# Optimization experiments

Measured on AMD Instinct MI355X. Metric: run time of the kernel, lower is better.

## Reference

```python
import jax, jax.numpy as jnp
import numpy as np

EPS = 1e-5

def layer_norm(x, g, b):
    m = x.mean(-1, keepdims=True)
    v = ((x - m) ** 2).mean(-1, keepdims=True)
    return (x - m) / jnp.sqrt(v + EPS) * g + b

def multihead(qn, kn, vn, Wq, Wk, Wv, causal):
    # Wq/Wk/Wv: [H, E, D]; per-head projections stacked over H (matches per-head Linear loop)
    Q = jnp.einsum('ble,hed->bhld', qn, Wq)
    K = jnp.einsum('bme,hed->bhmd', kn, Wk)
    V = jnp.einsum('bme,hed->bhmd', vn, Wv)
    scale = Q.shape[-1] ** -0.5
    s = jnp.einsum('bhld,bhmd->bhlm', Q, K) * scale
    if causal:
        L, M = s.shape[-2], s.shape[-1]
        mask = jnp.tril(jnp.ones((L, M), dtype=bool))
        s = jnp.where(mask, s, -jnp.inf)
    w = jax.nn.softmax(s, axis=-1)
    o = jnp.einsum('bhlm,bhmd->bhld', w, V)
    return o.mean(axis=1)  # heads are AVERAGED, not concatenated


def setup_inputs() -> dict:
    key = jax.random.key(0)
    ks = jax.random.split(key, 16)
    B, L, E, H, D, FW = 4, 2048, 512, 8, 512, 4
    std = 0.02
    inp = {
        'q': jax.random.normal(ks[0], (B, L, E), jnp.float32),
        'k': jax.random.normal(ks[1], (B, L, E), jnp.float32),
        'v': jax.random.normal(ks[2], (B, L, E), jnp.float32),
        'Wq_s': jax.random.normal(ks[3], (H, E, D), jnp.float32) * std,
        'Wk_s': jax.random.normal(ks[4], (H, E, D), jnp.float32) * std,
        'Wv_s': jax.random.normal(ks[5], (H, E, D), jnp.float32) * std,
        'Wq_c': jax.random.normal(ks[6], (H, E, D), jnp.float32) * std,
        'Wk_c': jax.random.normal(ks[7], (H, E, D), jnp.float32) * std,
        'Wv_c': jax.random.normal(ks[8], (H, E, D), jnp.float32) * std,
        'W1': jax.random.normal(ks[9], (E, FW * E), jnp.float32) * std,
        'b1': jnp.zeros((FW * E,), jnp.float32),
        'W2': jax.random.normal(ks[10], (FW * E, E), jnp.float32) * std,
        'b2': jnp.zeros((E,), jnp.float32),
        'g1': jnp.ones((E,), jnp.float32), 'be1': jnp.zeros((E,), jnp.float32),
        'g2': jnp.ones((E,), jnp.float32), 'be2': jnp.zeros((E,), jnp.float32),
        'g3': jnp.ones((E,), jnp.float32), 'be3': jnp.zeros((E,), jnp.float32),
    }
    return inp


def reference(q, k, v, Wq_s, Wk_s, Wv_s, Wq_c, Wk_c, Wv_c, W1, b1, W2, b2,
              g1, be1, g2, be2, g3, be3):
    # pre-norm causal self-attn (head_size == n_embd, heads averaged)
    q = q + multihead(layer_norm(q, g1, be1), layer_norm(q, g1, be1), layer_norm(q, g1, be1),
                      Wq_s, Wk_s, Wv_s, causal=True)
    # pre-norm cross-attn: only queries are normed; k, v used raw
    q = q + multihead(layer_norm(q, g2, be2), k, v, Wq_c, Wk_c, Wv_c, causal=False)
    # FFN
    h = layer_norm(q, g3, be3)
    h = jax.nn.relu(h @ W1 + b1) @ W2 + b2
    return q + h
```

## Files before the change

### kernel.cpp

```cpp
#include <hip/hip_runtime.h>
#include <cstdint>


typedef __bf16 bf16;
typedef __bf16 bf16x8 __attribute__((ext_vector_type(8)));
typedef float f32x4 __attribute__((ext_vector_type(4)));
typedef int i32x4 __attribute__((ext_vector_type(4)));
typedef int i32x8 __attribute__((ext_vector_type(8)));
typedef unsigned short u16;

static constexpr int Bb = 4, Ls = 2048, Es = 512, Hh = 8, Dd = 512, Ff = 2048;
static constexpr long BL = (long)Bb * Ls;
static constexpr int BIG = 1 << 30;

#define DEV __device__ __forceinline__

DEV u16 f2bf(float x) {
  unsigned u = __float_as_uint(x);
  return (u16)((u + 0x7fffu + ((u >> 16) & 1u)) >> 16);
}

DEV void async16(const void* gp, void* lp) {
  __builtin_amdgcn_global_load_lds(
      (const __attribute__((address_space(1))) void*)gp,
      (__attribute__((address_space(3))) void*)lp, 16, 0, 0);
}

template <int OUT, int SM, int IN8, int O8, bool BIAS, bool RELU, bool CAUSAL, bool RESID>
__global__ __launch_bounds__(256) void gemm128(
    const void* __restrict__ A, const void* __restrict__ Bt, void* __restrict__ Cout,
    const float* __restrict__ bias, const float* __restrict__ resid,
    float* __restrict__ rsum,
    int M, int N, int K, int lda, int ldb, int ldc, int ldct, int tz,
    long sA, int dA, long sAi, int mA, int dAi,
    long sB, int mB, long sB2, int dB,
    long sC, int dC, long sCi, int mC, float alpha) {
  const int m0 = blockIdx.y * 128, n0 = blockIdx.x * 128;
  if (CAUSAL && SM == 1 && n0 > m0 + 127) return;
  int Keff = K;
  if (CAUSAL && SM == 2) { int kl = m0 + 128; Keff = kl < K ? kl : K; }

  const int z = blockIdx.z;
  const char* Ab = (const char*)A + (long)(z / dA) * sA + (long)((z % mA) / dAi) * sAi;
  const char* Bbp = (const char*)Bt + (long)(z % mB) * sB + (long)(z / dB) * sB2;
  char* Cb = (char*)Cout + (long)(z / dC) * sC + (long)(z % mC) * sCi;
  float* RS = (SM != 0) ? (rsum + (long)z * M) : nullptr;
  const int zc = z % mC;

  constexpr int ES = IN8 ? 1 : 2;
  constexpr int KS = IN8 ? 128 : 64;
  const long lasA = (long)lda * ES, lasB = (long)ldb * ES;

  __shared__ char As[16384];
  __shared__ char Bs[16384];

  const int tid = threadIdx.x;
  const int lane = tid & 63;
  const int quad = lane >> 4, r = lane & 15;
  const int wave = tid >> 6;
  const int wm = (wave >> 1) * 64, wn = (wave & 1) * 64;

  f32x4 acc[4][4];
  const f32x4 zero = {0.f, 0.f, 0.f, 0.f};
#pragma unroll
  for (int i = 0; i < 4; ++i)
#pragma unroll
    for (int j = 0; j < 4; ++j) acc[i][j] = zero;

  for (int k0 = 0; k0 < Keff; k0 += KS) {
#pragma unroll
    for (int i = 0; i < 4; ++i) {
      const int c = i * 256 + tid, row = c >> 3;
      const int s = (c & 7) ^ (row & 7);
      async16(Ab + (long)(m0 + row) * lasA + ((long)k0 * ES + s * 16), As + c * 16);
    }
#pragma unroll
    for (int i = 0; i < 4; ++i) {
      const int c = i * 256 + tid, row = c >> 3;
      const int s = (c & 7) ^ (row & 7);
      async16(Bbp + (long)(n0 + row) * lasB + ((long)k0 * ES + s * 16), Bs + c * 16);
    }
    asm volatile("s_waitcnt vmcnt(0)" ::: "memory");
    __syncthreads();

    if (IN8) {
      i32x8 af[4], bw[4];
#pragma unroll
      for (int t = 0; t < 4; ++t) {
        const int Ra = wm + t * 16 + r;
        const char* pa = As + Ra * 128;
        i32x4 alo = *(const i32x4*)(pa + (((2 * quad) ^ (Ra & 7)) * 16));
        i32x4 ahi = *(const i32x4*)(pa + (((2 * quad + 1) ^ (Ra & 7)) * 16));
        af[t] = __builtin_shufflevector(alo, ahi, 0, 1, 2, 3, 4, 5, 6, 7);
        const int Rb = wn + t * 16 + r;
        const char* pb = Bs + Rb * 128;
        i32x4 blo = *(const i32x4*)(pb + (((2 * quad) ^ (Rb & 7)) * 16));
        i32x4 bhi = *(const i32x4*)(pb + (((2 * quad + 1) ^ (Rb & 7)) * 16));
        bw[t] = __builtin_shufflevector(blo, bhi, 0, 1, 2, 3, 4, 5, 6, 7);
      }
#pragma unroll
      for (int i = 0; i < 4; ++i)
#pragma unroll
        for (int j = 0; j < 4; ++j)
          acc[i][j] = __builtin_amdgcn_mfma_scale_f32_16x16x128_f8f6f4(
              af[i], bw[j], acc[i][j], 0, 0, 0, 0x7f7f7f7f, 0, 0x7f7f7f7f);
    } else {
#pragma unroll
      for (int u = 0; u < 2; ++u) {
        bf16x8 af[4], bw[4];
#pragma unroll
        for (int t = 0; t < 4; ++t) {
          const int Ra = wm + t * 16 + r;
          af[t] = *(const bf16x8*)(As + Ra * 128 + (((u * 4 + quad) ^ (Ra & 7)) * 16));
          const int Rb = wn + t * 16 + r;
          bw[t] = *(const bf16x8*)(Bs + Rb * 128 + (((u * 4 + quad) ^ (Rb & 7)) * 16));
        }
#pragma unroll
        for (int i = 0; i < 4; ++i)
#pragma unroll
          for (int j = 0; j < 4; ++j)
            acc[i][j] = __builtin_amdgcn_mfma_f32_16x16x32_bf16(af[i], bw[j], acc[i][j], 0, 0, 0);
      }
    }
    __syncthreads();
  }

#pragma unroll
  for (int i = 0; i < 4; ++i) {
    const int rowb = m0 + wm + i * 16 + quad * 4;
    if (SM == 1) {
      float rpart[4] = {0.f, 0.f, 0.f, 0.f};
#pragma unroll
      for (int j = 0; j < 4; ++j) {
        const int col = n0 + wn + j * 16 + r;
#pragma unroll
        for (int t = 0; t < 4; ++t) {
          float p = __expf(acc[i][j][t] * alpha);
          if (CAUSAL && col > rowb + t) p = 0.f;
          rpart[t] += p;
          if (O8) {
            int w8 = __builtin_amdgcn_cvt_pk_fp8_f32(p, p, 0, false);
            Cb[(long)(rowb + t) * ldc + col] = (char)(w8 & 0xff);
          } else {
            ((u16*)Cb)[(long)(rowb + t) * ldc + col] = f2bf(p);
          }
        }
      }
#pragma unroll
      for (int t = 0; t < 4; ++t) {
        rpart[t] += __shfl_xor(rpart[t], 1);
        rpart[t] += __shfl_xor(rpart[t], 2);
        rpart[t] += __shfl_xor(rpart[t], 4);
        rpart[t] += __shfl_xor(rpart[t], 8);
      }
      if (r == 0) {
#pragma unroll
        for (int t = 0; t < 4; ++t) atomicAdd(RS + rowb + t, rpart[t]);
      }
      continue;
    }
    float rinv[4];
    if (SM == 2) {
#pragma unroll
      for (int t = 0; t < 4; ++t) rinv[t] = alpha / RS[rowb + t];
    }
#pragma unroll
    for (int j = 0; j < 4; ++j) {
      const int col = n0 + wn + j * 16 + r;
      float v[4];
#pragma unroll
      for (int t = 0; t < 4; ++t)
        v[t] = (SM == 2) ? acc[i][j][t] * rinv[t] : acc[i][j][t] * alpha;
      if (BIAS) {
        const float bb = bias[col];
#pragma unroll
        for (int t = 0; t < 4; ++t) v[t] += bb;
      }
      if (RELU) {
#pragma unroll
        for (int t = 0; t < 4; ++t) v[t] = fmaxf(v[t], 0.f);
      }
      if (OUT == 0) {
        float* C = (float*)Cb;
#pragma unroll
        for (int t = 0; t < 4; ++t) {
          long idx = (long)(rowb + t) * ldc + col;
          float o = v[t];
          if (RESID) o += resid[idx];
          C[idx] = o;
        }
      } else {
        if (zc >= tz) {
          if (O8) {
            int w8 = __builtin_amdgcn_cvt_pk_fp8_f32(v[0], v[1], 0, false);
            w8 = __builtin_amdgcn_cvt_pk_fp8_f32(v[2], v[3], w8, true);
            *(int*)(Cb + (long)col * ldct + rowb) = w8;
          } else {
            ushort4 p;
            p.x = f2bf(v[0]); p.y = f2bf(v[1]); p.z = f2bf(v[2]); p.w = f2bf(v[3]);
            *(ushort4*)((u16*)Cb + (long)col * ldct + rowb) = p;
          }
        } else {
#pragma unroll
          for (int t = 0; t < 4; ++t) {
            if (O8) {
              int w8 = __builtin_amdgcn_cvt_pk_fp8_f32(v[t], v[t], 0, false);
              Cb[(long)(rowb + t) * ldc + col] = (char)(w8 & 0xff);
            } else {
              ((u16*)Cb)[(long)(rowb + t) * ldc + col] = f2bf(v[t]);
            }
          }
        }
      }
    }
  }
}

template <int F8>
__global__ __launch_bounds__(256) void ln_kernel(
    const float* __restrict__ x, const float* __restrict__ g, const float* __restrict__ be,
    void* __restrict__ y, float* __restrict__ xcopy, int nrows) {
  const int wave = threadIdx.x >> 6, lane = threadIdx.x & 63;
  const long row = (long)blockIdx.x * 4 + wave;
  const float4* xr = (const float4*)(x + row * 512);
  float4 v0 = xr[lane], v1 = xr[lane + 64];
  if (xcopy) {
    float4* c = (float4*)(xcopy + row * 512);
    c[lane] = v0; c[lane + 64] = v1;
  }
  float s = v0.x + v0.y + v0.z + v0.w + v1.x + v1.y + v1.z + v1.w;
#pragma unroll
  for (int o = 32; o >= 1; o >>= 1) s += __shfl_xor(s, o);
  const float m = s * (1.0f / 512.0f);
  float d = (v0.x - m) * (v0.x - m) + (v0.y - m) * (v0.y - m) + (v0.z - m) * (v0.z - m) +
            (v0.w - m) * (v0.w - m) + (v1.x - m) * (v1.x - m) + (v1.y - m) * (v1.y - m) +
            (v1.z - m) * (v1.z - m) + (v1.w - m) * (v1.w - m);
#pragma unroll
  for (int o = 32; o >= 1; o >>= 1) d += __shfl_xor(d, o);
  const float rstd = rsqrtf(d * (1.0f / 512.0f) + 1e-5f);
  const float4* gv = (const float4*)g;
  const float4* bv = (const float4*)be;
  float4 g0 = gv[lane], g1 = gv[lane + 64], b0 = bv[lane], b1 = bv[lane + 64];
  float n0 = (v0.x - m) * rstd * g0.x + b0.x, n1 = (v0.y - m) * rstd * g0.y + b0.y;
  float n2 = (v0.z - m) * rstd * g0.z + b0.z, n3 = (v0.w - m) * rstd * g0.w + b0.w;
  float n4 = (v1.x - m) * rstd * g1.x + b1.x, n5 = (v1.y - m) * rstd * g1.y + b1.y;
  float n6 = (v1.z - m) * rstd * g1.z + b1.z, n7 = (v1.w - m) * rstd * g1.w + b1.w;
  if (F8) {
    char* yr = (char*)y + row * 512;
    int w0 = __builtin_amdgcn_cvt_pk_fp8_f32(n0, n1, 0, false);
    w0 = __builtin_amdgcn_cvt_pk_fp8_f32(n2, n3, w0, true);
    int w1 = __builtin_amdgcn_cvt_pk_fp8_f32(n4, n5, 0, false);
    w1 = __builtin_amdgcn_cvt_pk_fp8_f32(n6, n7, w1, true);
    *(int*)(yr + 4 * lane) = w0;
    *(int*)(yr + 256 + 4 * lane) = w1;
  } else {
    uint2 o0, o1;
    o0.x = (unsigned)f2bf(n0) | ((unsigned)f2bf(n1) << 16);
    o0.y = (unsigned)f2bf(n2) | ((unsigned)f2bf(n3) << 16);
    o1.x = (unsigned)f2bf(n4) | ((unsigned)f2bf(n5) << 16);
    o1.y = (unsigned)f2bf(n6) | ((unsigned)f2bf(n7) << 16);
    uint2* yr = (uint2*)((u16*)y + row * 512);
    yr[lane] = o0; yr[lane + 64] = o1;
  }
}

__global__ __launch_bounds__(256) void cvt_fp8_kernel(const float* __restrict__ x,
                                                      char* __restrict__ y, long n) {
  long i = ((long)blockIdx.x * 256 + threadIdx.x) * 8;
  if (i >= n) return;
  float4 a = *(const float4*)(x + i), b = *(const float4*)(x + i + 4);
  int w0 = __builtin_amdgcn_cvt_pk_fp8_f32(a.x, a.y, 0, false);
  w0 = __builtin_amdgcn_cvt_pk_fp8_f32(a.z, a.w, w0, true);
  int w1 = __builtin_amdgcn_cvt_pk_fp8_f32(b.x, b.y, 0, false);
  w1 = __builtin_amdgcn_cvt_pk_fp8_f32(b.z, b.w, w1, true);
  int2 o; o.x = w0; o.y = w1;
  *(int2*)(y + i) = o;
}

__global__ __launch_bounds__(256) void zero_kernel(float* __restrict__ p) {
  long i = ((long)blockIdx.x * 256 + threadIdx.x) * 4;
  const float4 z4 = {0.f, 0.f, 0.f, 0.f};
  *(float4*)(p + i) = z4;
}

__global__ __launch_bounds__(256) void transpose6(
    const float* __restrict__ s0, const float* __restrict__ s1, const float* __restrict__ s2,
    const float* __restrict__ s3, const float* __restrict__ s4, const float* __restrict__ s5,
    char* __restrict__ out) {
  __shared__ float t[32][33];
  const int set = blockIdx.z >> 3, head = blockIdx.z & 7;
  const float* in = set == 0 ? s0 : set == 1 ? s1 : set == 2 ? s2
                   : set == 3 ? s3 : set == 4 ? s4 : s5;
  const long sW = (long)Es * Dd;
  in += (long)head * sW;
  char* o = out + ((long)set * Hh + head) * sW;
  const int c0 = blockIdx.x * 32, r0 = blockIdx.y * 32;
  const int tx = threadIdx.x & 31, ty = threadIdx.x >> 5;
#pragma unroll
  for (int i = 0; i < 32; i += 8) t[ty + i][tx] = in[(long)(r0 + ty + i) * Dd + (c0 + tx)];
  __syncthreads();
#pragma unroll
  for (int i = 0; i < 32; i += 8) {
    float xv = t[tx][ty + i] * 64.0f;
    o[(long)(c0 + ty + i) * Es + (r0 + tx)] =
        (char)(__builtin_amdgcn_cvt_pk_fp8_f32(xv, xv, 0, false) & 0xff);
  }
}

__global__ __launch_bounds__(256) void transpose_cvt(const float* __restrict__ in,
                                                     u16* __restrict__ out, int R, int C,
                                                     long sIn, long sOut) {
  __shared__ float t[32][33];
  in += (long)blockIdx.z * sIn;
  out += (long)blockIdx.z * sOut;
  const int c0 = blockIdx.x * 32, r0 = blockIdx.y * 32;
  const int tx = threadIdx.x & 31, ty = threadIdx.x >> 5;
#pragma unroll
  for (int i = 0; i < 32; i += 8) t[ty + i][tx] = in[(long)(r0 + ty + i) * C + (c0 + tx)];
  __syncthreads();
#pragma unroll
  for (int i = 0; i < 32; i += 8)
    out[(long)(c0 + ty + i) * R + (r0 + tx)] = f2bf(t[tx][ty + i]);
}

__global__ __launch_bounds__(256) void reduce8b_kernel(const u16* __restrict__ O,
                                                       float* __restrict__ acc) {
  const long n = (long)Ls * Dd;
  const u16* Ob = O + (long)blockIdx.y * 8 * n;
  float* ab = acc + (long)blockIdx.y * (long)Ls * Es;
  long i = ((long)blockIdx.x * 256 + threadIdx.x) * 8;
  float s[8] = {0.f, 0.f, 0.f, 0.f, 0.f, 0.f, 0.f, 0.f};
#pragma unroll
  for (int h = 0; h < 8; ++h) {
    bf16x8 t = *(const bf16x8*)(Ob + (long)h * n + i);
#pragma unroll
    for (int e = 0; e < 8; ++e) s[e] += (float)t[e];
  }
  float4 a0 = *(const float4*)(ab + i);
  float4 a1 = *(const float4*)(ab + i + 4);
  a0.x += s[0]; a0.y += s[1]; a0.z += s[2]; a0.w += s[3];
  a1.x += s[4]; a1.y += s[5]; a1.z += s[6]; a1.w += s[7];
  *(float4*)(ab + i) = a0;
  *(float4*)(ab + i + 4) = a1;
}

__global__ __launch_bounds__(256) void finalize_kernel(const float* __restrict__ slabs,
                                                       const float* __restrict__ resid,
                                                       const float* __restrict__ b2,
                                                       float* __restrict__ out) {
  const long SL = (long)BL * Es;
  long i = ((long)blockIdx.x * 256 + threadIdx.x) * 4;
  float4 a0 = *(const float4*)(slabs + i);
  float4 a1 = *(const float4*)(slabs + SL + i);
  float4 a2 = *(const float4*)(slabs + 2 * SL + i);
  float4 a3 = *(const float4*)(slabs + 3 * SL + i);
  float4 rr = *(const float4*)(resid + i);
  float4 bb = *(const float4*)(b2 + (int)(i & 511));
  float4 o;
  o.x = a0.x + a1.x + a2.x + a3.x + rr.x + bb.x;
  o.y = a0.y + a1.y + a2.y + a3.y + rr.y + bb.y;
  o.z = a0.z + a1.z + a2.z + a3.z + rr.z + bb.z;
  o.w = a0.w + a1.w + a2.w + a3.w + rr.w + bb.w;
  *(float4*)(out + i) = o;
}

extern "C" void kernel_launch(void* const* d_in, const int* in_sizes, int n_in,
                              void* d_out, int out_size, void* d_ws, size_t ws_size,
                              hipStream_t stream) {
  const float* q = (const float*)d_in[0];
  const float* k = (const float*)d_in[1];
  const float* v = (const float*)d_in[2];
  const float* Wq_s = (const float*)d_in[3];
  const float* Wk_s = (const float*)d_in[4];
  const float* Wv_s = (const float*)d_in[5];
  const float* Wq_c = (const float*)d_in[6];
  const float* Wk_c = (const float*)d_in[7];
  const float* Wv_c = (const float*)d_in[8];
  const float* W1 = (const float*)d_in[9];
  const float* b1 = (const float*)d_in[10];
  const float* W2 = (const float*)d_in[11];
  const float* b2 = (const float*)d_in[12];
  const float* g1 = (const float*)d_in[13];
  const float* be1 = (const float*)d_in[14];
  const float* g2 = (const float*)d_in[15];
  const float* be2 = (const float*)d_in[16];
  const float* g3 = (const float*)d_in[17];
  const float* be3 = (const float*)d_in[18];

  char* w = (char*)d_ws;
  size_t off = 0;
  auto alloc = [&](size_t bytes) -> char* {
    char* p = w + off;
    off += (bytes + 255) & ~(size_t)255;
    return p;
  };
  const long sW = (long)Es * Dd;
  const long sQ = (long)Ls * Dd;
  const long sS = (long)Ls * Ls;
  const long sBE = (long)Ls * Es;

  u16* Wqst = (u16*)alloc((size_t)Hh * sW * 2);
  u16* Wkst = (u16*)alloc((size_t)Hh * sW * 2);
  u16* Wvst = (u16*)alloc((size_t)Hh * sW * 2);
  u16* Wqct = (u16*)alloc((size_t)Hh * sW * 2);
  u16* Wkct = (u16*)alloc((size_t)Hh * sW * 2);
  u16* Wvct = (u16*)alloc((size_t)Hh * sW * 2);
  u16* W1t = (u16*)alloc((size_t)Es * Ff * 2);
  u16* W2t = (u16*)alloc((size_t)Es * Ff * 2);
  u16* qn = (u16*)alloc((size_t)BL * Es * 2);
  u16* knb = (u16*)alloc((size_t)BL * Es * 2);
  u16* vnb = (u16*)alloc((size_t)BL * Es * 2);
  char* QKV = alloc((size_t)Hh * sQ * 2);
  char* KVx = alloc((size_t)Hh * sQ * 2);
  u16* Vtb = (u16*)alloc((size_t)Hh * sQ * 2);
  char* Sb = alloc((size_t)Hh * sS * 2);
  float* acc1 = (float*)alloc((size_t)BL * Es * 4);
  u16* hbuf = (u16*)alloc((size_t)BL * Ff * 2);
  (void)KVx; (void)Vtb; (void)Wkst; (void)Wvst; (void)Wqct; (void)Wkct; (void)Wvct;
  char* QKVp = QKV;
  float* accF = (float*)Sb;
  float* rsum = (float*)W1t;
  char* Wq8 = (char*)Wqst;
  char* qn8 = (char*)qn;
  const long tstr = (long)BL * Es * 2;
  (void)in_sizes; (void)n_in; (void)out_size; (void)ws_size;

  const dim3 blk(256);
  transpose6<<<dim3(Dd / 32, Es / 32, 48), blk, 0, stream>>>(Wq_s, Wk_s, Wv_s, Wq_c, Wk_c, Wv_c, Wq8);
  cvt_fp8_kernel<<<dim3((unsigned)(BL * Es / 2048)), blk, 0, stream>>>(k, (char*)knb, BL * Es);
  cvt_fp8_kernel<<<dim3((unsigned)(BL * Es / 2048)), blk, 0, stream>>>(v, (char*)vnb, BL * Es);
  zero_kernel<<<dim3(8 * Hh * Ls / 1024), blk, 0, stream>>>(rsum);

  ln_kernel<1><<<dim3((unsigned)(BL / 4)), blk, 0, stream>>>(q, g1, be1, qn8, acc1, (int)BL);

  const float scl = 0.044194173824159216f;
  const float sclS = scl / 4096.0f;
  const float aPV = 0.125f / 64.0f;
  const float* np = nullptr;

  for (int p = 0; p < 2; ++p) {
    const char* qp8 = qn8 + (long)p * 2 * sBE;
    float* rsS = rsum + (long)p * 16 * Ls;
    gemm128<1, 0, 1, 1, false, false, false, false><<<dim3(4, 16, 48), blk, 0, stream>>>(
        qp8, Wq8, QKVp, np, np, nullptr, Ls, Dd, Es, Es, Es, Dd, Ls, 16,
        sBE, 24, 0, 24, 8,
        sW, 24, 0, 1,
        24 * sQ, 24, sQ, 24,
        1.0f);
    gemm128<1, 1, 1, 1, false, false, true, false><<<dim3(16, 16, 16), blk, 0, stream>>>(
        QKVp, QKVp + 8 * sQ, Sb, np, np, rsS, Ls, Ls, Dd, Dd, Dd, Ls, Ls, BIG,
        24 * sQ, 8, sQ, 8, 1,
        sQ, 8, 24 * sQ, 8,
        8 * sS, 8, sS, 8,
        sclS);
    gemm128<1, 2, 1, 0, false, false, true, false><<<dim3(4, 16, 16), blk, 0, stream>>>(
        Sb, QKVp + 16 * sQ, hbuf, np, np, rsS, Ls, Dd, Ls, Ls, Ls, Dd, Ls, BIG,
        8 * sS, 8, sS, 8, 1,
        sQ, 8, 24 * sQ, 8,
        8 * sQ * 2, 8, sQ * 2, 8,
        aPV);
    reduce8b_kernel<<<dim3(512, 2), blk, 0, stream>>>(hbuf, acc1 + (long)p * 2 * sBE);
  }

  ln_kernel<1><<<dim3((unsigned)(BL / 4)), blk, 0, stream>>>(acc1, g2, be2, qn8, nullptr, (int)BL);

  for (int p = 0; p < 2; ++p) {
    const char* qp8 = qn8 + (long)p * 2 * sBE;
    float* rsS = rsum + (long)(32 + p * 16) * Ls;
    gemm128<1, 0, 1, 1, false, false, false, false><<<dim3(4, 16, 48), blk, 0, stream>>>(
        qp8, Wq8 + 24 * sW, QKVp, np, np, nullptr, Ls, Dd, Es, Es, Es, Dd, Ls, 16,
        sBE, 24, tstr, 24, 8,
        sW, 24, 0, 1,
        24 * sQ, 24, sQ, 24,
        1.0f);
    gemm128<1, 1, 1, 1, false, false, false, false><<<dim3(16, 16, 16), blk, 0, stream>>>(
        QKVp, QKVp + 8 * sQ, Sb, np, np, rsS, Ls, Ls, Dd, Dd, Dd, Ls, Ls, BIG,
        24 * sQ, 8, sQ, 8, 1,
        sQ, 8, 24 * sQ, 8,
        8 * sS, 8, sS, 8,
        sclS);
    gemm128<1, 2, 1, 0, false, false, false, false><<<dim3(4, 16, 16), blk, 0, stream>>>(
        Sb, QKVp + 16 * sQ, hbuf, np, np, rsS, Ls, Dd, Ls, Ls, Ls, Dd, Ls, BIG,
        8 * sS, 8, sS, 8, 1,
        sQ, 8, 24 * sQ, 8,
        8 * sQ * 2, 8, sQ * 2, 8,
        aPV);
    reduce8b_kernel<<<dim3(512, 2), blk, 0, stream>>>(hbuf, acc1 + (long)p * 2 * sBE);
  }

  transpose_cvt<<<dim3(Ff / 32, Es / 32, 1), blk, 0, stream>>>(W1, W1t, Es, Ff, 0, 0);
  transpose_cvt<<<dim3(Es / 32, Ff / 32, 1), blk, 0, stream>>>(W2, W2t, Ff, Es, 0, 0);

  ln_kernel<0><<<dim3((unsigned)(BL / 4)), blk, 0, stream>>>(acc1, g3, be3, qn, nullptr, (int)BL);
  gemm128<1, 0, 0, 0, true, true, false, false><<<dim3(Ff / 128, (unsigned)(BL / 128), 1), blk, 0, stream>>>(
      qn, W1t, hbuf, b1, np, nullptr, (int)BL, Ff, Es, Es, Es, Ff, Ff, BIG,
      0, 1, 0, 1, 1,
      0, 1, 0, 1,
      0, 1, 0, 1, 1.0f);
  gemm128<0, 0, 0, 0, false, false, false, false><<<dim3(Es / 128, (unsigned)(BL / 128), 4), blk, 0, stream>>>(
      hbuf, W2t, accF, np, np, nullptr, (int)BL, Es, 512, Ff, Ff, Es, Es, BIG,
      1024, 1, 0, 1, 1,
      0, 1, 1024, 1,
      (long)BL * Es * 4, 1, 0, 1,
      1.0f);
  finalize_kernel<<<dim3((unsigned)(BL * Es / 1024)), blk, 0, stream>>>(accF, acc1, b2, (float*)d_out);
}
```

Baseline: 925.8 us.

## Run FFN GEMMs in FP8 and launch causal score GEMM on triangular grid

The FFN weights are now transposed and converted to scaled FP8 instead of bf16. The FFN layer norm and both FFN GEMMs now take FP8 inputs with a 1/64 output scale, which halves operand bytes and uses the faster FP8 matrix path. The causal self-attention score GEMM is also launched over a 1D triangular grid of 136 tiles per batch-head, so blocks that would only exit early are never launched. FP8 activations and weights in the FFN lower numeric precision and could hurt accuracy.

```diff
diff --git a/kernel.cpp b/kernel.cpp
--- a/kernel.cpp
+++ b/kernel.cpp
@@ -26,7 +26,8 @@
       (__attribute__((address_space(3))) void*)lp, 16, 0, 0);
 }
 
-template <int OUT, int SM, int IN8, int O8, bool BIAS, bool RELU, bool CAUSAL, bool RESID>
+template <int OUT, int SM, int IN8, int O8, bool BIAS, bool RELU, bool CAUSAL, bool RESID,
+          bool TRI>
 __global__ __launch_bounds__(256) void gemm128(
     const void* __restrict__ A, const void* __restrict__ Bt, void* __restrict__ Cout,
     const float* __restrict__ bias, const float* __restrict__ resid,
@@ -35,8 +36,18 @@
     long sA, int dA, long sAi, int mA, int dAi,
     long sB, int mB, long sB2, int dB,
     long sC, int dC, long sCi, int mC, float alpha) {
-  const int m0 = blockIdx.y * 128, n0 = blockIdx.x * 128;
-  if (CAUSAL && SM == 1 && n0 > m0 + 127) return;
+  int xt, yt;
+  if (TRI) {
+    const int bx = blockIdx.x;
+    int y = (int)((sqrtf(8.0f * bx + 1.0f) - 1.0f) * 0.5f);
+    while ((y + 1) * (y + 2) / 2 <= bx) ++y;
+    while (y * (y + 1) / 2 > bx) --y;
+    yt = y; xt = bx - y * (y + 1) / 2;
+  } else {
+    xt = blockIdx.x; yt = blockIdx.y;
+  }
+  const int m0 = yt * 128, n0 = xt * 128;
+  if (!TRI && CAUSAL && SM == 1 && n0 > m0 + 127) return;
   int Keff = K;
   if (CAUSAL && SM == 2) { int kl = m0 + 128; Keff = kl < K ? kl : K; }
 
@@ -307,20 +318,20 @@
   }
 }
 
-__global__ __launch_bounds__(256) void transpose_cvt(const float* __restrict__ in,
-                                                     u16* __restrict__ out, int R, int C,
-                                                     long sIn, long sOut) {
+__global__ __launch_bounds__(256) void transpose_cvt8(const float* __restrict__ in,
+                                                      char* __restrict__ out, int R, int C) {
   __shared__ float t[32][33];
-  in += (long)blockIdx.z * sIn;
-  out += (long)blockIdx.z * sOut;
   const int c0 = blockIdx.x * 32, r0 = blockIdx.y * 32;
   const int tx = threadIdx.x & 31, ty = threadIdx.x >> 5;
 #pragma unroll
   for (int i = 0; i < 32; i += 8) t[ty + i][tx] = in[(long)(r0 + ty + i) * C + (c0 + tx)];
   __syncthreads();
 #pragma unroll
-  for (int i = 0; i < 32; i += 8)
-    out[(long)(c0 + ty + i) * R + (r0 + tx)] = f2bf(t[tx][ty + i]);
+  for (int i = 0; i < 32; i += 8) {
+    float xv = t[tx][ty + i] * 64.0f;
+    out[(long)(c0 + ty + i) * R + (r0 + tx)] =
+        (char)(__builtin_amdgcn_cvt_pk_fp8_f32(xv, xv, 0, false) & 0xff);
+  }
 }
 
 __global__ __launch_bounds__(256) void reduce8b_kernel(const u16* __restrict__ O,
@@ -422,6 +433,9 @@
   float* rsum = (float*)W1t;
   char* Wq8 = (char*)Wqst;
   char* qn8 = (char*)qn;
+  char* W1t8 = (char*)W1t;
+  char* W2t8 = (char*)W2t;
+  char* h8 = (char*)hbuf;
   const long tstr = (long)BL * Es * 2;
   (void)in_sizes; (void)n_in; (void)out_size; (void)ws_size;
 
@@ -436,24 +450,25 @@
   const float scl = 0.044194173824159216f;
   const float sclS = scl / 4096.0f;
   const float aPV = 0.125f / 64.0f;
+  const float aW = 1.0f / 64.0f;
   const float* np = nullptr;
 
   for (int p = 0; p < 2; ++p) {
     const char* qp8 = qn8 + (long)p * 2 * sBE;
     float* rsS = rsum + (long)p * 16 * Ls;
-    gemm128<1, 0, 1, 1, false, false, false, false><<<dim3(4, 16, 48), blk, 0, stream>>>(
+    gemm128<1, 0, 1, 1, false, false, false, false, false><<<dim3(4, 16, 48), blk, 0, stream>>>(
         qp8, Wq8, QKVp, np, np, nullptr, Ls, Dd, Es, Es, Es, Dd, Ls, 16,
         sBE, 24, 0, 24, 8,
         sW, 24, 0, 1,
         24 * sQ, 24, sQ, 24,
         1.0f);
-    gemm128<1, 1, 1, 1, false, false, true, false><<<dim3(16, 16, 16), blk, 0, stream>>>(
+    gemm128<1, 1, 1, 1, false, false, true, false, true><<<dim3(136, 1, 16), blk, 0, stream>>>(
         QKVp, QKVp + 8 * sQ, Sb, np, np, rsS, Ls, Ls, Dd, Dd, Dd, Ls, Ls, BIG,
         24 * sQ, 8, sQ, 8, 1,
         sQ, 8, 24 * sQ, 8,
         8 * sS, 8, sS, 8,
         sclS);
-    gemm128<1, 2, 1, 0, false, false, true, false><<<dim3(4, 16, 16), blk, 0, stream>>>(
+    gemm128<1, 2, 1, 0, false, false, true, false, false><<<dim3(4, 16, 16), blk, 0, stream>>>(
         Sb, QKVp + 16 * sQ, hbuf, np, np, rsS, Ls, Dd, Ls, Ls, Ls, Dd, Ls, BIG,
         8 * sS, 8, sS, 8, 1,
         sQ, 8, 24 * sQ, 8,
@@ -467,19 +482,19 @@
   for (int p = 0; p < 2; ++p) {
     const char* qp8 = qn8 + (long)p * 2 * sBE;
     float* rsS = rsum + (long)(32 + p * 16) * Ls;
-    gemm128<1, 0, 1, 1, false, false, false, false><<<dim3(4, 16, 48), blk, 0, stream>>>(
+    gemm128<1, 0, 1, 1, false, false, false, false, false><<<dim3(4, 16, 48), blk, 0, stream>>>(
         qp8, Wq8 + 24 * sW, QKVp, np, np, nullptr, Ls, Dd, Es, Es, Es, Dd, Ls, 16,
         sBE, 24, tstr, 24, 8,
         sW, 24, 0, 1,
         24 * sQ, 24, sQ, 24,
         1.0f);
-    gemm128<1, 1, 1, 1, false, false, false, false><<<dim3(16, 16, 16), blk, 0, stream>>>(
+    gemm128<1, 1, 1, 1, false, false, false, false, false><<<dim3(16, 16, 16), blk, 0, stream>>>(
         QKVp, QKVp + 8 * sQ, Sb, np, np, rsS, Ls, Ls, Dd, Dd, Dd, Ls, Ls, BIG,
         24 * sQ, 8, sQ, 8, 1,
         sQ, 8, 24 * sQ, 8,
         8 * sS, 8, sS, 8,
         sclS);
-    gemm128<1, 2, 1, 0, false, false, false, false><<<dim3(4, 16, 16), blk, 0, stream>>>(
+    gemm128<1, 2, 1, 0, false, false, false, false, false><<<dim3(4, 16, 16), blk, 0, stream>>>(
         Sb, QKVp + 16 * sQ, hbuf, np, np, rsS, Ls, Dd, Ls, Ls, Ls, Dd, Ls, BIG,
         8 * sS, 8, sS, 8, 1,
         sQ, 8, 24 * sQ, 8,
@@ -488,20 +503,20 @@
     reduce8b_kernel<<<dim3(512, 2), blk, 0, stream>>>(hbuf, acc1 + (long)p * 2 * sBE);
   }
 
-  transpose_cvt<<<dim3(Ff / 32, Es / 32, 1), blk, 0, stream>>>(W1, W1t, Es, Ff, 0, 0);
-  transpose_cvt<<<dim3(Es / 32, Ff / 32, 1), blk, 0, stream>>>(W2, W2t, Ff, Es, 0, 0);
-
-  ln_kernel<0><<<dim3((unsigned)(BL / 4)), blk, 0, stream>>>(acc1, g3, be3, qn, nullptr, (int)BL);
-  gemm128<1, 0, 0, 0, true, true, false, false><<<dim3(Ff / 128, (unsigned)(BL / 128), 1), blk, 0, stream>>>(
-      qn, W1t, hbuf, b1, np, nullptr, (int)BL, Ff, Es, Es, Es, Ff, Ff, BIG,
+  transpose_cvt8<<<dim3(Ff / 32, Es / 32, 1), blk, 0, stream>>>(W1, W1t8, Es, Ff);
+  transpose_cvt8<<<dim3(Es / 32, Ff / 32, 1), blk, 0, stream>>>(W2, W2t8, Ff, Es);
+
+  ln_kernel<1><<<dim3((unsigned)(BL / 4)), blk, 0, stream>>>(acc1, g3, be3, qn8, nullptr, (int)BL);
+  gemm128<1, 0, 1, 1, true, true, false, false, false><<<dim3(Ff / 128, (unsigned)(BL / 128), 1), blk, 0, stream>>>(
+      qn8, W1t8, h8, b1, np, nullptr, (int)BL, Ff, Es, Es, Es, Ff, Ff, BIG,
       0, 1, 0, 1, 1,
       0, 1, 0, 1,
-      0, 1, 0, 1, 1.0f);
-  gemm128<0, 0, 0, 0, false, false, false, false><<<dim3(Es / 128, (unsigned)(BL / 128), 4), blk, 0, stream>>>(
-      hbuf, W2t, accF, np, np, nullptr, (int)BL, Es, 512, Ff, Ff, Es, Es, BIG,
-      1024, 1, 0, 1, 1,
-      0, 1, 1024, 1,
+      0, 1, 0, 1, aW);
+  gemm128<0, 0, 1, 0, false, false, false, false, false><<<dim3(Es / 128, (unsigned)(BL / 128), 4), blk, 0, stream>>>(
+      h8, W2t8, accF, np, np, nullptr, (int)BL, Es, 512, Ff, Ff, Es, Es, BIG,
+      512, 1, 0, 1, 1,
+      0, 1, 512, 1,
       (long)BL * Es * 4, 1, 0, 1,
-      1.0f);
+      aW);
   finalize_kernel<<<dim3((unsigned)(BL * Es / 1024)), blk, 0, stream>>>(accF, acc1, b2, (float*)d_out);
 }
```

Result: faster. 891.6 us (-3.7%).
